# Kernel tuning notes

Measured on AMD Instinct MI355X. Metric: run time of the kernel, lower is better.

## Reference

```python
import jax, jax.numpy as jnp
import numpy as np

SR = 16000
FRAME_LENGTH = 2048
HOP = 512
WIN_LENGTH = 30
FREQ_LOW = 85
FREQ_HIGH = 3400
EPS = 1e-9


def setup_inputs() -> dict:
    key = jax.random.key(0)
    waveform = jax.random.normal(key, (8, 960000), dtype=jnp.float32)
    return {"waveform": waveform}


def _detect_pitch(w):
    # w: [B, T] padded waveform. Mirrors torchaudio.functional.detect_pitch_frequency.
    B, T = w.shape
    frame_size = int(np.ceil(SR * (HOP / SR)))          # = HOP = 512
    lags = int(np.ceil(SR / FREQ_LOW))                  # 189
    num_frames = int(np.ceil(T / frame_size))
    p = lags + num_frames * frame_size - T
    wp = jnp.pad(w, ((0, 0), (0, p)))                   # [B, lags + F*fs]
    frames = wp[:, : num_frames * frame_size].reshape(B, num_frames, frame_size)
    s1n = (EPS + jnp.linalg.norm(frames, axis=-1)) ** 2  # [B, F], lag-independent

    def body(carry, lag):
        seg = jax.lax.dynamic_slice_in_dim(wp, lag, num_frames * frame_size, axis=1)
        seg = seg.reshape(B, num_frames, frame_size)
        num = jnp.sum(frames * seg, axis=-1)
        s2n = (EPS + jnp.linalg.norm(seg, axis=-1)) ** 2
        return carry, num / s1n / s2n

    _, nccf = jax.lax.scan(body, None, jnp.arange(1, lags + 1))  # [lags, B, F]
    nccf = jnp.moveaxis(nccf, 0, -1)                             # [B, F, lags]

    # _find_max_per_frame
    lag_min = int(np.ceil(SR / FREQ_HIGH))  # 5
    half_size = lags // 2                   # 94
    best_v = jnp.max(nccf[..., lag_min:], axis=-1)
    best_i = jnp.argmax(nccf[..., lag_min:], axis=-1)
    half_v = jnp.max(nccf[..., lag_min:half_size], axis=-1)
    half_i = jnp.argmax(nccf[..., lag_min:half_size], axis=-1)
    mask = half_v > 0.99 * best_v           # prefer near-max with smallest lag
    idx = jnp.where(mask, half_i, best_i) + lag_min + 1  # +1 calibration offset

    # lower median (sorted index (n-1)//2). Output length = F - (WIN_LENGTH-1-pad_len).
    pad_len = (WIN_LENGTH - 1) // 2         # 14
    padded = jnp.concatenate([jnp.tile(idx[:, :1], (1, pad_len)), idx], axis=-1)
    out_len = padded.shape[-1] - WIN_LENGTH + 1
    win_idx = jnp.arange(out_len)[:, None] + jnp.arange(WIN_LENGTH)[None, :]
    wins = padded[:, win_idx]               # [B, out_len, WIN_LENGTH]
    med = jnp.sort(wins, axis=-1)[..., (WIN_LENGTH - 1) // 2]

    return SR / (EPS + med.astype(jnp.float32))


def reference(waveform):
    pad = FRAME_LENGTH // 2
    wpad = jnp.pad(waveform, ((0, 0), (pad, pad)), mode="reflect")
    pitch = _detect_pitch(wpad)
    desired = waveform.shape[-1] // HOP + 1
    if pitch.shape[-1] > desired:
        pitch = pitch[..., :desired]
    else:
        pitch = jnp.pad(pitch, ((0, 0), (0, desired - pitch.shape[-1])))
    return pitch
```

## Files before the change

kernel.cpp:

```cpp
#include <hip/hip_runtime.h>

#define T_WPAD  962048
#define T_RAW   960000
#define NFRM    1879
#define OUTW    1876
#define MEDLEN  1864
#define WINL    30
#define PADL    14
#define FPB     8
#define NBX     235
#define XLEN    4296
#define X4LEN   1074

#define NCCF_BODY(O, AUSE, ALOAD, KEXPR, QOUT, DO_LOAD_A, DO_STORE_W)           \
    {                                                                           \
        if (DO_LOAD_A) ALOAD = X4[aK + (KEXPR) + 1];                            \
        float4 nx;                                                              \
        if (DO_STORE_W) nx = X4[wBase + (KEXPR) + 4];                           \
        _Pragma("unroll")                                                       \
        for (int r = 0; r < 12; ++r) {                                          \
            acc[r] = fmaf(AUSE.x, w[(O + r + 1) & 15], acc[r]);                 \
            acc[r] = fmaf(AUSE.y, w[(O + r + 2) & 15], acc[r]);                 \
            acc[r] = fmaf(AUSE.z, w[(O + r + 3) & 15], acc[r]);                 \
            acc[r] = fmaf(AUSE.w, w[(O + r + 4) & 15], acc[r]);                 \
        }                                                                       \
        if (DO_STORE_W) {                                                       \
            QOUT = fmaf(nx.x, nx.x, fmaf(nx.y, nx.y, fmaf(nx.z, nx.z, nx.w * nx.w))); \
            w[(O + 0) & 15] = nx.x; w[(O + 1) & 15] = nx.y;                     \
            w[(O + 2) & 15] = nx.z; w[(O + 3) & 15] = nx.w;                     \
        }                                                                       \
    }

__global__ __launch_bounds__(128) void nccf_kernel(const float* __restrict__ wav,
                                                   int* __restrict__ idxArr) {
    const int bx   = blockIdx.x;
    const int b    = blockIdx.y;
    const int tid  = threadIdx.x;
    const int wave = tid >> 6;
    const int lane = tid & 63;
    const int g    = lane >> 4;
    const int s    = lane & 15;

    __shared__ __align__(16) float X[XLEN];

    const long a0 = (long)bx * (FPB * 512);
    const float* wrow = wav + (long)b * T_RAW;

    if (bx >= 1 && bx <= NBX - 2) {
        const float4* src = (const float4*)(wrow + (a0 - 1024));
        float4* dst = (float4*)X;
        for (int i = tid; i < X4LEN; i += 128) dst[i] = src[i];
    } else {
        for (int i = tid; i < XLEN; i += 128) {
            float v = 0.0f;
            long t = a0 + i;
            if (t < T_WPAD) {
                long u = t - 1024;
                if (u < 0) u = -u;
                if (u >= T_RAW) u = 2L * (T_RAW - 1) - u;
                v = wrow[u];
            }
            X[i] = v;
        }
    }
    __syncthreads();

    const int F  = wave * 4 + g;
    const int gf = bx * FPB + F;
    const bool valid = (gf < NFRM);

    float acc[12];
    #pragma unroll
    for (int r = 0; r < 12; ++r) acc[r] = 0.0f;
    float sq[12];
    double Tcur = 0.0;
    double T512 = 0.0;
    float w[16];

    {
        const float4* X4 = (const float4*)X;
        const int aK    = F * 128;
        const int wBase = aK + 3 * s;

        #pragma unroll
        for (int d = 0; d < 4; ++d) {
            float4 t4 = X4[wBase + d];
            w[4 * d] = t4.x; w[4 * d + 1] = t4.y; w[4 * d + 2] = t4.z; w[4 * d + 3] = t4.w;
        }
        #pragma unroll
        for (int j = 0; j < 12; ++j) sq[j] = w[j] * w[j];
        #pragma unroll
        for (int j = 0; j < 16; ++j) Tcur += (double)(w[j] * w[j]);

        float4 Aev = X4[aK];
        float4 Aod;
        float q0, q1, q2, q3;

        #pragma unroll 2
        for (int kg = 0; kg < 31; ++kg) {
            const int k4 = kg * 4;
            NCCF_BODY(0,  Aev, Aod, k4 + 0, q0, true, true)
            NCCF_BODY(4,  Aod, Aev, k4 + 1, q1, true, true)
            NCCF_BODY(8,  Aev, Aod, k4 + 2, q2, true, true)
            NCCF_BODY(12, Aod, Aev, k4 + 3, q3, true, true)
            Tcur += (double)((q0 + q1) + (q2 + q3));
        }
        T512 = Tcur;

        NCCF_BODY(0,  Aev, Aod, 124, q0, true,  true)
        NCCF_BODY(4,  Aod, Aev, 125, q1, true,  true)
        NCCF_BODY(8,  Aev, Aod, 126, q2, true,  true)
        NCCF_BODY(12, Aod, Aod, 127, q3, false, false)
    }

    double qv[12];
    {
        double Thi = T512, Tlo = 0.0;
        #pragma unroll
        for (int r = 1; r <= 12; ++r) {
            float eh = w[r - 1];
            Thi += (double)(eh * eh);
            Tlo += (double)sq[r - 1];
            qv[r - 1] = Thi - Tlo;
        }
    }
    double s1d = __shfl(T512, 0, 16);

    float bestv = -1e30f, halfv = -1e30f;
    int bestk = 1 << 30, halfk = 1 << 30;
    {
        float s1 = 1e-9f + sqrtf((float)s1d);
        float s1n = s1 * s1;
        #pragma unroll
        for (int r = 1; r <= 12; ++r) {
            int lag  = 12 * s + r;
            int kidx = lag - 1;
            if (kidx <= 188) {
                float s2 = 1e-9f + sqrtf((float)qv[r - 1]);
                float v  = acc[r - 1] / s1n / (s2 * s2);
                if (kidx >= 5) {
                    if (v > bestv) { bestv = v; bestk = kidx; }
                    if (kidx <= 93 && v > halfv) { halfv = v; halfk = kidx; }
                }
            }
        }
    }

    #pragma unroll
    for (int off = 8; off >= 1; off >>= 1) {
        float ov = __shfl_xor(bestv, off, 16); int ok = __shfl_xor(bestk, off, 16);
        if (ov > bestv || (ov == bestv && ok < bestk)) { bestv = ov; bestk = ok; }
        float hv = __shfl_xor(halfv, off, 16); int hk = __shfl_xor(halfk, off, 16);
        if (hv > halfv || (hv == halfv && hk < halfk)) { halfv = hv; halfk = hk; }
    }

    if (valid && s == 0) {
        bool m = (halfv > 0.99f * bestv);
        int sel = m ? halfk : bestk;
        idxArr[b * NFRM + gf] = sel + 1;
    }
}

__global__ __launch_bounds__(256) void med_kernel(const int* __restrict__ idxArr,
                                                  float* __restrict__ out) {
    int gid = blockIdx.x * 256 + threadIdx.x;
    if (gid >= 8 * OUTW) return;
    int b = gid / OUTW;
    int i = gid - b * OUTW;
    float o = 0.0f;
    if (i < MEDLEN) {
        const int* row = idxArr + b * NFRM;
        int vals[WINL];
        #pragma unroll
        for (int m = 0; m < WINL; ++m) {
            int sIdx = i + m - PADL;
            vals[m] = row[sIdx < 0 ? 0 : sIdx];
        }
        int med = vals[0];
        #pragma unroll
        for (int c = 0; c < WINL; ++c) {
            int cl = 0, ce = 0;
            #pragma unroll
            for (int m = 0; m < WINL; ++m) {
                cl += (vals[m] <  vals[c]) ? 1 : 0;
                ce += (vals[m] == vals[c]) ? 1 : 0;
            }
            if (cl <= 14 && 14 < cl + ce) med = vals[c];
        }
        o = 16000.0f / (1e-9f + (float)med);
    }
    out[gid] = o;
}

extern "C" void kernel_launch(void* const* d_in, const int* in_sizes, int n_in,
                              void* d_out, int out_size, void* d_ws, size_t ws_size,
                              hipStream_t stream) {
    const float* wav = (const float*)d_in[0];
    float* out = (float*)d_out;
    int* idxArr = (int*)d_ws;

    dim3 gB(NBX, 8);
    hipLaunchKernelGGL(nccf_kernel, gB, dim3(128), 0, stream, wav, idxArr);

    int total = 8 * OUTW;
    hipLaunchKernelGGL(med_kernel, dim3((total + 255) / 256), dim3(256), 0, stream,
                       idxArr, out);
}
```

Baseline: 66.14 us.

## Shrink NCCF blocks to one wave and compute energies via parallel scan

```diff
diff --git a/kernel.cpp b/kernel.cpp
--- a/kernel.cpp
+++ b/kernel.cpp
@@ -7,16 +7,15 @@
 #define MEDLEN  1864
 #define WINL    30
 #define PADL    14
-#define FPB     8
-#define NBX     235
-#define XLEN    4296
-#define X4LEN   1074
-
-#define NCCF_BODY(O, AUSE, ALOAD, KEXPR, QOUT, DO_LOAD_A, DO_STORE_W)           \
+#define FPB     4
+#define NBX     470
+#define XLEN    2244
+#define X4LEN   561
+
+#define NCCF_BODY(O, AUSE, ALOAD, K)                                            \
     {                                                                           \
-        if (DO_LOAD_A) ALOAD = X4[aK + (KEXPR) + 1];                            \
-        float4 nx;                                                              \
-        if (DO_STORE_W) nx = X4[wBase + (KEXPR) + 4];                           \
+        ALOAD = X4[aK + (K) + 1];                                               \
+        float4 nx = X4[wBase + (K) + 4];                                        \
         _Pragma("unroll")                                                       \
         for (int r = 0; r < 12; ++r) {                                          \
             acc[r] = fmaf(AUSE.x, w[(O + r + 1) & 15], acc[r]);                 \
@@ -24,19 +23,15 @@
             acc[r] = fmaf(AUSE.z, w[(O + r + 3) & 15], acc[r]);                 \
             acc[r] = fmaf(AUSE.w, w[(O + r + 4) & 15], acc[r]);                 \
         }                                                                       \
-        if (DO_STORE_W) {                                                       \
-            QOUT = fmaf(nx.x, nx.x, fmaf(nx.y, nx.y, fmaf(nx.z, nx.z, nx.w * nx.w))); \
-            w[(O + 0) & 15] = nx.x; w[(O + 1) & 15] = nx.y;                     \
-            w[(O + 2) & 15] = nx.z; w[(O + 3) & 15] = nx.w;                     \
-        }                                                                       \
-    }
-
-__global__ __launch_bounds__(128) void nccf_kernel(const float* __restrict__ wav,
-                                                   int* __restrict__ idxArr) {
+        w[(O + 0) & 15] = nx.x; w[(O + 1) & 15] = nx.y;                         \
+        w[(O + 2) & 15] = nx.z; w[(O + 3) & 15] = nx.w;                         \
+    }
+
+__global__ __launch_bounds__(64) void nccf_kernel(const float* __restrict__ wav,
+                                                  int* __restrict__ idxArr) {
     const int bx   = blockIdx.x;
     const int b    = blockIdx.y;
     const int tid  = threadIdx.x;
-    const int wave = tid >> 6;
     const int lane = tid & 63;
     const int g    = lane >> 4;
     const int s    = lane & 15;
@@ -49,9 +44,9 @@
     if (bx >= 1 && bx <= NBX - 2) {
         const float4* src = (const float4*)(wrow + (a0 - 1024));
         float4* dst = (float4*)X;
-        for (int i = tid; i < X4LEN; i += 128) dst[i] = src[i];
+        for (int i = tid; i < X4LEN; i += 64) dst[i] = src[i];
     } else {
-        for (int i = tid; i < XLEN; i += 128) {
+        for (int i = tid; i < XLEN; i += 64) {
             float v = 0.0f;
             long t = a0 + i;
             if (t < T_WPAD) {
@@ -65,71 +60,84 @@
     }
     __syncthreads();
 
-    const int F  = wave * 4 + g;
+    const int F  = g;
     const int gf = bx * FPB + F;
     const bool valid = (gf < NFRM);
 
+    const float4* X4 = (const float4*)X;
+    const int aK    = F * 128;
+    const int wBase = aK + 3 * s;
+
+    double T0 = 0.0;
+    {
+        const float4* fb = X4 + aK + 8 * s;
+        #pragma unroll
+        for (int m = 0; m < 8; ++m) {
+            float4 v4 = fb[m];
+            T0 += (double)v4.x * v4.x; T0 += (double)v4.y * v4.y;
+            T0 += (double)v4.z * v4.z; T0 += (double)v4.w * v4.w;
+        }
+        #pragma unroll
+        for (int off = 8; off >= 1; off >>= 1) T0 += __shfl_xor(T0, off, 16);
+    }
+
     float acc[12];
     #pragma unroll
     for (int r = 0; r < 12; ++r) acc[r] = 0.0f;
     float sq[12];
-    double Tcur = 0.0;
-    double T512 = 0.0;
     float w[16];
-
-    {
-        const float4* X4 = (const float4*)X;
-        const int aK    = F * 128;
-        const int wBase = aK + 3 * s;
-
+    float4 Aev, Aod;
+
+    {
         #pragma unroll
         for (int d = 0; d < 4; ++d) {
             float4 t4 = X4[wBase + d];
-            w[4 * d] = t4.x; w[4 * d + 1] = t4.y; w[4 * d + 2] = t4.z; w[4 * d + 3] = t4.w;
+            w[4*d] = t4.x; w[4*d+1] = t4.y; w[4*d+2] = t4.z; w[4*d+3] = t4.w;
         }
         #pragma unroll
         for (int j = 0; j < 12; ++j) sq[j] = w[j] * w[j];
-        #pragma unroll
-        for (int j = 0; j < 16; ++j) Tcur += (double)(w[j] * w[j]);
-
-        float4 Aev = X4[aK];
-        float4 Aod;
-        float q0, q1, q2, q3;
-
-        #pragma unroll 2
-        for (int kg = 0; kg < 31; ++kg) {
-            const int k4 = kg * 4;
-            NCCF_BODY(0,  Aev, Aod, k4 + 0, q0, true, true)
-            NCCF_BODY(4,  Aod, Aev, k4 + 1, q1, true, true)
-            NCCF_BODY(8,  Aev, Aod, k4 + 2, q2, true, true)
-            NCCF_BODY(12, Aod, Aev, k4 + 3, q3, true, true)
-            Tcur += (double)((q0 + q1) + (q2 + q3));
-        }
-        T512 = Tcur;
-
-        NCCF_BODY(0,  Aev, Aod, 124, q0, true,  true)
-        NCCF_BODY(4,  Aod, Aev, 125, q1, true,  true)
-        NCCF_BODY(8,  Aev, Aod, 126, q2, true,  true)
-        NCCF_BODY(12, Aod, Aod, 127, q3, false, false)
-    }
+        Aev = X4[aK];
+    }
+
+    #pragma unroll 2
+    for (int kg = 0; kg < 32; ++kg) {
+        const int k4 = kg * 4;
+        NCCF_BODY(0,  Aev, Aod, k4 + 0)
+        NCCF_BODY(4,  Aod, Aev, k4 + 1)
+        NCCF_BODY(8,  Aev, Aod, k4 + 2)
+        NCCF_BODY(12, Aod, Aev, k4 + 3)
+    }
+
+    double Lsum = 0.0, Rsum = 0.0;
+    #pragma unroll
+    for (int j = 0; j < 12; ++j) {
+        Lsum += (double)sq[j];
+        Rsum += (double)w[j] * w[j];
+    }
+    double D = Rsum - Lsum, inc = D;
+    #pragma unroll
+    for (int off = 1; off < 16; off <<= 1) {
+        double v = __shfl_up(inc, off, 16);
+        if (s >= off) inc += v;
+    }
+    const double Ts = T0 + (inc - D);
 
     double qv[12];
     {
-        double Thi = T512, Tlo = 0.0;
+        double Thi = Ts, Tlo = 0.0;
         #pragma unroll
         for (int r = 1; r <= 12; ++r) {
             float eh = w[r - 1];
-            Thi += (double)(eh * eh);
+            Thi += (double)eh * eh;
             Tlo += (double)sq[r - 1];
             qv[r - 1] = Thi - Tlo;
         }
     }
-    double s1d = __shfl(T512, 0, 16);
 
     float bestv = -1e30f, halfv = -1e30f;
     int bestk = 1 << 30, halfk = 1 << 30;
     {
-        float s1 = 1e-9f + sqrtf((float)s1d);
+        float s1 = 1e-9f + sqrtf((float)T0);
         float s1n = s1 * s1;
         #pragma unroll
         for (int r = 1; r <= 12; ++r) {
@@ -200,7 +208,7 @@
     int* idxArr = (int*)d_ws;
 
     dim3 gB(NBX, 8);
-    hipLaunchKernelGGL(nccf_kernel, gB, dim3(128), 0, stream, wav, idxArr);
+    hipLaunchKernelGGL(nccf_kernel, gB, dim3(64), 0, stream, wav, idxArr);
 
     int total = 8 * OUTW;
     hipLaunchKernelGGL(med_kernel, dim3((total + 255) / 256), dim3(256), 0, stream,
```

Measured after the change: 61.90 us. -6.4%, faster.
